# Optimization experiments

Measured on AMD Instinct MI355X. Metric: run time of the kernel, lower is better.

## Reference

```python
import jax, jax.numpy as jnp
import numpy as np

N_NODES = 50000
N_EDGES = 800000
D_IN = 128
D_H = 128
D_SIG = 16
D_OUT = 128


def _linear_params(key, fan_in, fan_out):
    kw, kb = jax.random.split(key)
    bound = 1.0 / np.sqrt(fan_in)
    w = jax.random.uniform(kw, (fan_in, fan_out), jnp.float32, -bound, bound)
    b = jax.random.uniform(kb, (fan_out,), jnp.float32, -bound, bound)
    return w, b


def setup_inputs() -> dict:
    key = jax.random.key(0)
    ks = jax.random.split(key, 7)
    x = jax.random.normal(ks[0], (N_NODES, D_IN), jnp.float32)
    edge_index = jax.random.randint(ks[1], (2, N_EDGES), 0, N_NODES, jnp.int64 if jax.config.jax_enable_x64 else jnp.int32)
    enc_w, enc_b = _linear_params(ks[2], D_IN, D_H)
    sig_w, sig_b = _linear_params(ks[3], D_H, D_SIG)
    msg_w, msg_b = _linear_params(ks[4], D_H, D_H)
    agg_w, agg_b = _linear_params(ks[5], 2 * D_H, D_H)
    dec_w, dec_b = _linear_params(ks[6], D_H, D_OUT)
    return {"x": x, "edge_index": edge_index,
            "enc_w": enc_w, "enc_b": enc_b,
            "sig_w": sig_w, "sig_b": sig_b,
            "msg_w": msg_w, "msg_b": msg_b,
            "agg_w": agg_w, "agg_b": agg_b,
            "dec_w": dec_w, "dec_b": dec_b}


def reference(x, edge_index, enc_w, enc_b, sig_w, sig_b, msg_w, msg_b, agg_w, agg_b, dec_w, dec_b):
    n = x.shape[0]
    h = x @ enc_w + enc_b                                   # [N, D_H]
    sig = h @ sig_w + sig_b                                 # [N, D_SIG]
    # F.normalize: x / max(||x||_2, eps)
    sig = sig / jnp.maximum(jnp.linalg.norm(sig, axis=-1, keepdims=True), 1e-12)
    msg = jax.nn.relu(h @ msg_w + msg_b)                    # [N, D_H]

    src, dst = edge_index[0], edge_index[1]
    # per-edge signature dot product, then segment softmax over each src node's edges
    scores = jnp.sum(sig[src] * sig[dst], axis=-1)          # [E]
    smax = jax.ops.segment_max(scores, src, num_segments=n)
    smax = jnp.where(jnp.isfinite(smax), smax, 0.0)         # empty segments -> 0
    e = jnp.exp(scores - smax[src])
    denom = jax.ops.segment_sum(e, src, num_segments=n)
    w = e / denom[src]                                      # [E]
    # weighted message aggregation; nodes with no out-edges get zeros
    comm = jax.ops.segment_sum(w[:, None] * msg[dst], src, num_segments=n)  # [N, D_H]

    combined = jax.nn.relu(jnp.concatenate([h, comm], axis=-1) @ agg_w + agg_b)
    return combined @ dec_w + dec_b
```

## Files before the change

### kernel.cpp

```cpp
#include <hip/hip_runtime.h>
#include <math.h>

#define N_NODES 50000
#define N_EDGES 800000
#define CAP 64
#define NRANGE 782
#define PCAP 1280
#define EPBA 2560
#define NBA 313
#define NBE 391

typedef __attribute__((ext_vector_type(8)))  short s16x8;
typedef __attribute__((ext_vector_type(16))) float f32x16;
typedef unsigned int u32;
typedef unsigned short u16;

union U16B { uint4 u; s16x8 s; };

__device__ __forceinline__ u32 bfr(float f) {
    u32 u = __float_as_uint(f);
    return (u + 0x7FFFu + ((u >> 16) & 1u)) >> 16;
}
__device__ __forceinline__ u32 pkbf(float a, float b) { return bfr(a) | (bfr(b) << 16); }
__device__ __forceinline__ float bf2f(u32 b) { return __uint_as_float(b << 16); }
__device__ __forceinline__ float dotpair(u32 a, u32 b) {
    return bf2f(a & 0xFFFFu) * bf2f(b & 0xFFFFu) + bf2f(a >> 16) * bf2f(b >> 16);
}

__device__ __forceinline__ uint4 buildfrag(const float* d8, int hh) {
    u32 P = pkbf(d8[0], d8[1]), Q = pkbf(d8[2], d8[3]);
    u32 R = pkbf(d8[4], d8[5]), S = pkbf(d8[6], d8[7]);
    u32 sP = (u32)__shfl_xor((int)P, 32);
    u32 sQ = (u32)__shfl_xor((int)Q, 32);
    u32 sR = (u32)__shfl_xor((int)R, 32);
    u32 sS = (u32)__shfl_xor((int)S, 32);
    uint4 f;
    f.x = hh ? sR : P;  f.y = hh ? sS : Q;
    f.z = hh ? R : sP;  f.w = hh ? S : sQ;
    return f;
}
#define BUILDF(OUT, ACC, Q, HH) do { \
    float _td[8]; \
    _Pragma("unroll") for (int _z = 0; _z < 8; ++_z) _td[_z] = (ACC)[(Q)*8 + _z]; \
    (OUT) = buildfrag(_td, HH); } while (0)
#define BUILDR(OUT, ACC, Q, HH) do { \
    float _td[8]; \
    _Pragma("unroll") for (int _z = 0; _z < 8; ++_z) _td[_z] = fmaxf((ACC)[(Q)*8 + _z], 0.f); \
    (OUT) = buildfrag(_td, HH); } while (0)

__global__ __launch_bounds__(256) void k_prep(
    const float* __restrict__ enc_w, const float* __restrict__ msg_w,
    const float* __restrict__ sig_w, const float* __restrict__ agg_w,
    const float* __restrict__ dec_w,
    uint4* __restrict__ WtE, uint4* __restrict__ WtM, uint4* __restrict__ WtD,
    uint4* __restrict__ WtA0, uint4* __restrict__ WtA1, uint4* __restrict__ WtS,
    int* __restrict__ gcur)
{
    int gid = blockIdx.x * 256 + threadIdx.x;
    if (gid < NRANGE) gcur[gid] = 0;
    if (gid < 10240) {
        int m = gid >> 11, r = gid & 2047;
        int col = r >> 4, s = r & 15;
        const float* W; uint4* D; int kb = 0;
        if      (m == 0) { W = enc_w; D = WtE; }
        else if (m == 1) { W = msg_w; D = WtM; }
        else if (m == 2) { W = dec_w; D = WtD; }
        else if (m == 3) { W = agg_w; D = WtA0; }
        else             { W = agg_w; D = WtA1; kb = 128; }
        float v[8];
        #pragma unroll
        for (int j = 0; j < 8; ++j) v[j] = W[(size_t)(kb + s * 8 + j) * 128 + col];
        uint4 w;
        w.x = pkbf(v[0], v[1]); w.y = pkbf(v[2], v[3]);
        w.z = pkbf(v[4], v[5]); w.w = pkbf(v[6], v[7]);
        D[col * 16 + (s ^ (col & 7))] = w;
    } else if (gid < 10752) {
        int r = gid - 10240;
        int row = r >> 4, s = r & 15;
        float v[8];
        #pragma unroll
        for (int j = 0; j < 8; ++j)
            v[j] = (row < 16) ? sig_w[(size_t)(s * 8 + j) * 16 + row] : 0.0f;
        uint4 w;
        w.x = pkbf(v[0], v[1]); w.y = pkbf(v[2], v[3]);
        w.z = pkbf(v[4], v[5]); w.w = pkbf(v[6], v[7]);
        WtS[row * 16 + (s ^ (row & 7))] = w;
    }
}

__global__ __launch_bounds__(256) void k_enc_part(
    const float* __restrict__ x,
    const uint4* __restrict__ WtE, const uint4* __restrict__ WtM,
    const uint4* __restrict__ WtS,
    const float* __restrict__ enc_b, const float* __restrict__ sig_b,
    const float* __restrict__ msg_b,
    uint4* __restrict__ h_g, u32* __restrict__ sig_bf, uint4* __restrict__ msg_g,
    const int* __restrict__ src, const int* __restrict__ dst,
    int* __restrict__ gcur, u32* __restrict__ part)
{
    __shared__ uint4 LB[2048];
    __shared__ float LS[2176];

    const int t = threadIdx.x;

    if (blockIdx.x >= NBE) {
        int* hist = (int*)LB;
        int* base = hist + NRANGE;
        const int e0 = (blockIdx.x - NBE) * EPBA;
        for (int i = t; i < NRANGE; i += 256) hist[i] = 0;
        __syncthreads();
        #pragma unroll 4
        for (int k = 0; k < EPBA / 256; ++k) {
            int e = e0 + k * 256 + t;
            if (e < N_EDGES) atomicAdd(&hist[src[e] >> 6], 1);
        }
        __syncthreads();
        for (int i = t; i < NRANGE; i += 256) {
            int h = hist[i];
            base[i] = h ? atomicAdd(&gcur[i], h) : 0;
        }
        __syncthreads();
        for (int i = t; i < NRANGE; i += 256) hist[i] = 0;
        __syncthreads();
        #pragma unroll 4
        for (int k = 0; k < EPBA / 256; ++k) {
            int e = e0 + k * 256 + t;
            if (e < N_EDGES) {
                int s = src[e], d = dst[e];
                int r = s >> 6;
                int p = base[r] + atomicAdd(&hist[r], 1);
                part[(size_t)r * PCAP + p] = ((u32)s << 16) | (u32)d;
            }
        }
        return;
    }

    const int node0 = blockIdx.x * 128;
    int nrem = N_NODES - node0; if (nrem > 128) nrem = 128;
    const int lane = t & 63, wid = t >> 6;
    const int l31 = lane & 31, hh = lane >> 5;
    const int nloc = wid * 32 + l31;
    const int sw7 = l31 & 7;

    #pragma unroll
    for (int it = 0; it < 8; ++it) {
        int idx = it * 256 + t;
        int nd = idx >> 4, s = idx & 15;
        float4 v0 = make_float4(0, 0, 0, 0), v1 = v0;
        if (nd < nrem) {
            const float4* px = (const float4*)(x + (size_t)(node0 + nd) * 128 + s * 8);
            v0 = px[0]; v1 = px[1];
        }
        uint4 w;
        w.x = pkbf(v0.x, v0.y); w.y = pkbf(v0.z, v0.w);
        w.z = pkbf(v1.x, v1.y); w.w = pkbf(v1.z, v1.w);
        LB[nd * 16 + (s ^ (nd & 7))] = w;
    }
    __syncthreads();

    const char* lb = (const char*)LB;
    const char* gwE = (const char*)WtE;
    const char* gwM = (const char*)WtM;
    const char* gwS = (const char*)WtS;

    f32x16 a0 = {}, a1 = {}, a2 = {}, a3 = {};
    #pragma unroll
    for (int r = 0; r < 16; ++r) {
        int rr = (r & 3) + 8 * (r >> 2) + 4 * hh;
        a0[r] = enc_b[rr];      a1[r] = enc_b[32 + rr];
        a2[r] = enc_b[64 + rr]; a3[r] = enc_b[96 + rr];
    }
    #pragma unroll
    for (int ks = 0; ks < 8; ++ks) {
        int so = ((ks * 2 + hh) ^ sw7) << 4;
        s16x8 bf = *(const s16x8*)(lb + nloc * 256 + so);
        s16x8 w0 = *(const s16x8*)(gwE + l31 * 256 + so);
        s16x8 w1 = *(const s16x8*)(gwE + 8192 + l31 * 256 + so);
        s16x8 w2 = *(const s16x8*)(gwE + 16384 + l31 * 256 + so);
        s16x8 w3 = *(const s16x8*)(gwE + 24576 + l31 * 256 + so);
        a0 = __builtin_amdgcn_mfma_f32_32x32x16_bf16(w0, bf, a0, 0, 0, 0);
        a1 = __builtin_amdgcn_mfma_f32_32x32x16_bf16(w1, bf, a1, 0, 0, 0);
        a2 = __builtin_amdgcn_mfma_f32_32x32x16_bf16(w2, bf, a2, 0, 0, 0);
        a3 = __builtin_amdgcn_mfma_f32_32x32x16_bf16(w3, bf, a3, 0, 0, 0);
    }

    uint4 hf[8];
    BUILDF(hf[0], a0, 0, hh); BUILDF(hf[1], a0, 1, hh);
    BUILDF(hf[2], a1, 0, hh); BUILDF(hf[3], a1, 1, hh);
    BUILDF(hf[4], a2, 0, hh); BUILDF(hf[5], a2, 1, hh);
    BUILDF(hf[6], a3, 0, hh); BUILDF(hf[7], a3, 1, hh);

    __syncthreads();
    #pragma unroll
    for (int f = 0; f < 8; ++f) {
        int g = 2 * f + hh;
        LB[nloc * 16 + (g ^ sw7)] = hf[f];
    }

    f32x16 m0 = {}, m1 = {}, m2 = {}, m3 = {};
    #pragma unroll
    for (int r = 0; r < 16; ++r) {
        int rr = (r & 3) + 8 * (r >> 2) + 4 * hh;
        m0[r] = msg_b[rr];      m1[r] = msg_b[32 + rr];
        m2[r] = msg_b[64 + rr]; m3[r] = msg_b[96 + rr];
    }
    #pragma unroll
    for (int ks = 0; ks < 8; ++ks) {
        int so = ((ks * 2 + hh) ^ sw7) << 4;
        U16B hb; hb.u = hf[ks];
        s16x8 w0 = *(const s16x8*)(gwM + l31 * 256 + so);
        s16x8 w1 = *(const s16x8*)(gwM + 8192 + l31 * 256 + so);
        s16x8 w2 = *(const s16x8*)(gwM + 16384 + l31 * 256 + so);
        s16x8 w3 = *(const s16x8*)(gwM + 24576 + l31 * 256 + so);
        m0 = __builtin_amdgcn_mfma_f32_32x32x16_bf16(w0, hb.s, m0, 0, 0, 0);
        m1 = __builtin_amdgcn_mfma_f32_32x32x16_bf16(w1, hb.s, m1, 0, 0, 0);
        m2 = __builtin_amdgcn_mfma_f32_32x32x16_bf16(w2, hb.s, m2, 0, 0, 0);
        m3 = __builtin_amdgcn_mfma_f32_32x32x16_bf16(w3, hb.s, m3, 0, 0, 0);
    }
    uint4 mf[8];
    BUILDR(mf[0], m0, 0, hh); BUILDR(mf[1], m0, 1, hh);
    BUILDR(mf[2], m1, 0, hh); BUILDR(mf[3], m1, 1, hh);
    BUILDR(mf[4], m2, 0, hh); BUILDR(mf[5], m2, 1, hh);
    BUILDR(mf[6], m3, 0, hh); BUILDR(mf[7], m3, 1, hh);

    __syncthreads();
    #pragma unroll
    for (int it = 0; it < 8; ++it) {
        int idx = it * 256 + t;
        if ((idx >> 4) < nrem) h_g[(size_t)node0 * 16 + idx] = LB[idx];
    }
    __syncthreads();
    #pragma unroll
    for (int f = 0; f < 8; ++f)
        LB[nloc * 16 + 2 * f + hh] = mf[f];

    f32x16 sg = {};
    #pragma unroll
    for (int r = 0; r < 8; ++r) {
        int rr = (r & 3) + 8 * (r >> 2) + 4 * hh;
        sg[r] = sig_b[rr];
    }
    #pragma unroll
    for (int ks = 0; ks < 8; ++ks) {
        int so = ((ks * 2 + hh) ^ sw7) << 4;
        s16x8 aw = *(const s16x8*)(gwS + l31 * 256 + so);
        U16B hb; hb.u = hf[ks];
        sg = __builtin_amdgcn_mfma_f32_32x32x16_bf16(aw, hb.s, sg, 0, 0, 0);
    }
    float ss = 0.f;
    #pragma unroll
    for (int r = 0; r < 8; ++r) ss += sg[r] * sg[r];
    ss += __shfl_xor(ss, 32);
    float inv = 1.0f / fmaxf(sqrtf(ss), 1e-12f);
    #pragma unroll
    for (int r = 0; r < 8; ++r) {
        int sc = (r & 3) + 8 * (r >> 2) + 4 * hh;
        LS[nloc * 17 + sc] = sg[r] * inv;
    }
    __syncthreads();

    #pragma unroll
    for (int it = 0; it < 8; ++it) {
        int idx = it * 256 + t;
        if ((idx >> 4) < nrem) msg_g[(size_t)node0 * 16 + idx] = LB[idx];
    }
    #pragma unroll
    for (int it = 0; it < 4; ++it) {
        int idx = it * 256 + t;
        int nd = idx >> 3, c2 = idx & 7;
        if (nd < nrem)
            sig_bf[(size_t)(node0 + nd) * 8 + c2] =
                pkbf(LS[nd * 17 + 2 * c2], LS[nd * 17 + 2 * c2 + 1]);
    }
}

__global__ __launch_bounds__(256) void k_decode_m(
    const uint4* __restrict__ h_g, const uint4* __restrict__ comm,
    const uint4* __restrict__ WtA0, const uint4* __restrict__ WtA1,
    const uint4* __restrict__ WtD,
    const float* __restrict__ agg_b, const float* __restrict__ dec_b,
    float* __restrict__ out)
{
    __shared__ uint4 LB[2048];
    __shared__ uint4 LW[2048];

    const int t = threadIdx.x;
    const int node0 = blockIdx.x * 64;
    int nrem = N_NODES - node0; if (nrem > 64) nrem = 64;
    const int lane = t & 63, wid = t >> 6;
    const int l31 = lane & 31, hh = lane >> 5;
    const int ng = wid & 1, cp = wid >> 1;
    const int nloc = ng * 32 + l31;
    const int sw7 = l31 & 7;

    #pragma unroll
    for (int it = 0; it < 8; ++it) {
        int idx = it * 256 + t;
        int nd = idx >> 5, g = idx & 31;
        uint4 v = make_uint4(0, 0, 0, 0);
        if (nd < nrem)
            v = (g < 16) ? h_g[(size_t)(node0 + nd) * 16 + g]
                         : comm[(size_t)(node0 + nd) * 16 + (g - 16)];
        LB[nd * 32 + g] = v;
        LW[idx] = WtA0[idx];
    }
    __syncthreads();

    const char* lb = (const char*)LB;
    const char* lw = (const char*)LW;

    f32x16 c0 = {}, c1 = {};
    #pragma unroll
    for (int r = 0; r < 16; ++r) {
        int rr = (r & 3) + 8 * (r >> 2) + 4 * hh;
        c0[r] = agg_b[cp * 64 + rr];
        c1[r] = agg_b[cp * 64 + 32 + rr];
    }
    #pragma unroll
    for (int ks = 0; ks < 8; ++ks) {
        int so = ((ks * 2 + hh) ^ sw7) << 4;
        s16x8 bf = *(const s16x8*)(lb + nloc * 512 + so);
        s16x8 w0 = *(const s16x8*)(lw + (cp * 64 + l31) * 256 + so);
        s16x8 w1 = *(const s16x8*)(lw + (cp * 64 + 32 + l31) * 256 + so);
        c0 = __builtin_amdgcn_mfma_f32_32x32x16_bf16(w0, bf, c0, 0, 0, 0);
        c1 = __builtin_amdgcn_mfma_f32_32x32x16_bf16(w1, bf, c1, 0, 0, 0);
    }
    __syncthreads();
    #pragma unroll
    for (int it = 0; it < 8; ++it) LW[it * 256 + t] = WtA1[it * 256 + t];
    __syncthreads();
    #pragma unroll
    for (int ks = 8; ks < 16; ++ks) {
        int so = ((ks * 2 + hh) ^ sw7) << 4;
        int so2 = (((ks - 8) * 2 + hh) ^ sw7) << 4;
        s16x8 bf = *(const s16x8*)(lb + nloc * 512 + so);
        s16x8 w0 = *(const s16x8*)(lw + (cp * 64 + l31) * 256 + so2);
        s16x8 w1 = *(const s16x8*)(lw + (cp * 64 + 32 + l31) * 256 + so2);
        c0 = __builtin_amdgcn_mfma_f32_32x32x16_bf16(w0, bf, c0, 0, 0, 0);
        c1 = __builtin_amdgcn_mfma_f32_32x32x16_bf16(w1, bf, c1, 0, 0, 0);
    }
    __syncthreads();

    {
        uint4 cf[4];
        BUILDR(cf[0], c0, 0, hh); BUILDR(cf[1], c0, 1, hh);
        BUILDR(cf[2], c1, 0, hh); BUILDR(cf[3], c1, 1, hh);
        #pragma unroll
        for (int f = 0; f < 4; ++f) {
            int g = (cp * 4 + f) * 2 + hh;
            LB[nloc * 16 + (g ^ sw7)] = cf[f];
        }
    }
    #pragma unroll
    for (int it = 0; it < 8; ++it) LW[it * 256 + t] = WtD[it * 256 + t];
    __syncthreads();

    f32x16 o0 = {}, o1 = {};
    {
        float b0 = dec_b[cp * 64 + l31], b1 = dec_b[cp * 64 + 32 + l31];
        #pragma unroll
        for (int r = 0; r < 16; ++r) { o0[r] = b0; o1[r] = b1; }
    }
    #pragma unroll
    for (int ks = 0; ks < 8; ++ks) {
        int so = ((ks * 2 + hh) ^ sw7) << 4;
        s16x8 af = *(const s16x8*)(lb + nloc * 256 + so);
        s16x8 w0 = *(const s16x8*)(lw + (cp * 64 + l31) * 256 + so);
        s16x8 w1 = *(const s16x8*)(lw + (cp * 64 + 32 + l31) * 256 + so);
        o0 = __builtin_amdgcn_mfma_f32_32x32x16_bf16(af, w0, o0, 0, 0, 0);
        o1 = __builtin_amdgcn_mfma_f32_32x32x16_bf16(af, w1, o1, 0, 0, 0);
    }
    #pragma unroll
    for (int r = 0; r < 16; ++r) {
        int nd = ng * 32 + (r & 3) + 8 * (r >> 2) + 4 * hh;
        if (nd < nrem) {
            float* row = out + (size_t)(node0 + nd) * 128 + cp * 64;
            row[l31]      = o0[r];
            row[32 + l31] = o1[r];
        }
    }
}

__global__ __launch_bounds__(256) void k_pb_aggr(
    const int* __restrict__ gcur, const u32* __restrict__ part,
    const u32* __restrict__ sig_bf,
    const char* __restrict__ msg_g, char* __restrict__ comm)
{
    __shared__ int   cnt[64];
    __shared__ float lden[64];
    __shared__ int2  lde[64 * CAP];

    const int t = threadIdx.x;
    const int r = blockIdx.x;
    const int node0 = r * 64;

    if (t < 64) { cnt[t] = 0; lden[t] = 0.f; }
    __syncthreads();

    const int total = gcur[r];
    for (int i = t; i < total; i += 256) {
        u32 en = part[(size_t)r * PCAP + i];
        int s = (int)(en >> 16), d = (int)(en & 0xFFFFu);
        const uint4* ps = (const uint4*)(sig_bf + (size_t)s * 8);
        const uint4* pd = (const uint4*)(sig_bf + (size_t)d * 8);
        uint4 sa = ps[0], sb = ps[1];
        uint4 da = pd[0], db = pd[1];
        float dot = dotpair(sa.x, da.x) + dotpair(sa.y, da.y)
                  + dotpair(sa.z, da.z) + dotpair(sa.w, da.w)
                  + dotpair(sb.x, db.x) + dotpair(sb.y, db.y)
                  + dotpair(sb.z, db.z) + dotpair(sb.w, db.w);
        float e = __expf(dot);
        int sl = s & 63;
        int p = atomicAdd(&cnt[sl], 1);
        lde[sl * CAP + p] = make_int2(d, __float_as_int(e));
        atomicAdd(&lden[sl], e);
    }
    __syncthreads();

    const int lane = t & 63, wid = t >> 6;
    const int l31 = lane & 31, hh = lane >> 5;
    #pragma unroll
    for (int g = 0; g < 8; ++g) {
        const int nloc = wid * 16 + 2 * g + hh;
        const int node = node0 + nloc;
        const int cn = cnt[nloc];
        const int2* ld = &lde[nloc * CAP];
        float a0 = 0.f, a1 = 0.f, a2 = 0.f, a3 = 0.f;
        int k = 0;
        for (; k + 4 <= cn; k += 4) {
            int2 d0 = ld[k], d1 = ld[k + 1], d2 = ld[k + 2], d3 = ld[k + 3];
            uint2 m0 = *(const uint2*)(msg_g + (size_t)d0.x * 256 + 8 * l31);
            uint2 m1 = *(const uint2*)(msg_g + (size_t)d1.x * 256 + 8 * l31);
            uint2 m2 = *(const uint2*)(msg_g + (size_t)d2.x * 256 + 8 * l31);
            uint2 m3 = *(const uint2*)(msg_g + (size_t)d3.x * 256 + 8 * l31);
            float e0 = __int_as_float(d0.y), e1 = __int_as_float(d1.y);
            float e2 = __int_as_float(d2.y), e3 = __int_as_float(d3.y);
            a0 += e0 * bf2f(m0.x & 0xFFFFu); a1 += e0 * bf2f(m0.x >> 16);
            a2 += e0 * bf2f(m0.y & 0xFFFFu); a3 += e0 * bf2f(m0.y >> 16);
            a0 += e1 * bf2f(m1.x & 0xFFFFu); a1 += e1 * bf2f(m1.x >> 16);
            a2 += e1 * bf2f(m1.y & 0xFFFFu); a3 += e1 * bf2f(m1.y >> 16);
            a0 += e2 * bf2f(m2.x & 0xFFFFu); a1 += e2 * bf2f(m2.x >> 16);
            a2 += e2 * bf2f(m2.y & 0xFFFFu); a3 += e2 * bf2f(m2.y >> 16);
            a0 += e3 * bf2f(m3.x & 0xFFFFu); a1 += e3 * bf2f(m3.x >> 16);
            a2 += e3 * bf2f(m3.y & 0xFFFFu); a3 += e3 * bf2f(m3.y >> 16);
        }
        for (; k < cn; ++k) {
            int2 de = ld[k];
            float e = __int_as_float(de.y);
            uint2 m = *(const uint2*)(msg_g + (size_t)de.x * 256 + 8 * l31);
            a0 += e * bf2f(m.x & 0xFFFFu);
            a1 += e * bf2f(m.x >> 16);
            a2 += e * bf2f(m.y & 0xFFFFu);
            a3 += e * bf2f(m.y >> 16);
        }
        float den = lden[nloc];
        float inv = (den > 0.f) ? (1.0f / den) : 0.f;
        if (node < N_NODES) {
            uint2 w;
            w.x = pkbf(a0 * inv, a1 * inv);
            w.y = pkbf(a2 * inv, a3 * inv);
            *(uint2*)(comm + (size_t)node * 256 + ((8 * l31) ^ ((node & 7) << 4))) = w;
        }
    }
}

extern "C" void kernel_launch(void* const* d_in, const int* in_sizes, int n_in,
                              void* d_out, int out_size, void* d_ws, size_t ws_size,
                              hipStream_t stream)
{
    const float* x     = (const float*)d_in[0];
    const int*   ei    = (const int*)  d_in[1];
    const float* enc_w = (const float*)d_in[2];
    const float* enc_b = (const float*)d_in[3];
    const float* sig_w = (const float*)d_in[4];
    const float* sig_b = (const float*)d_in[5];
    const float* msg_w = (const float*)d_in[6];
    const float* msg_b = (const float*)d_in[7];
    const float* agg_w = (const float*)d_in[8];
    const float* agg_b = (const float*)d_in[9];
    const float* dec_w = (const float*)d_in[10];
    const float* dec_b = (const float*)d_in[11];
    float* out = (float*)d_out;

    const int* src = ei;
    const int* dst = ei + N_EDGES;

    char* p = (char*)d_ws;
    uint4* h_g   = (uint4*)p;  p += (size_t)N_NODES * 256;
    uint4* msg_g = (uint4*)p;  p += (size_t)N_NODES * 256;
    uint4* comm  = (uint4*)p;  p += (size_t)N_NODES * 256;
    u32*   sig_bf = (u32*)p;   p += (size_t)N_NODES * 32;
    u32*   part   = (u32*)p;   p += (size_t)NRANGE * PCAP * 4;
    int*   gcur   = (int*)p;   p += 4096;
    uint4* WtE  = (uint4*)p; p += 32768;
    uint4* WtM  = (uint4*)p; p += 32768;
    uint4* WtD  = (uint4*)p; p += 32768;
    uint4* WtA0 = (uint4*)p; p += 32768;
    uint4* WtA1 = (uint4*)p; p += 32768;
    uint4* WtS  = (uint4*)p; p += 8192;

    k_prep<<<42, 256, 0, stream>>>(enc_w, msg_w, sig_w, agg_w, dec_w,
                                   WtE, WtM, WtD, WtA0, WtA1, WtS, gcur);
    k_enc_part<<<NBE + NBA, 256, 0, stream>>>(
        x, WtE, WtM, WtS, enc_b, sig_b, msg_b, h_g, sig_bf, msg_g,
        src, dst, gcur, part);
    k_pb_aggr<<<NRANGE, 256, 0, stream>>>(
        gcur, part, sig_bf, (const char*)msg_g, (char*)comm);
    k_decode_m<<<(N_NODES + 63) / 64, 256, 0, stream>>>(
        h_g, comm, WtA0, WtA1, WtD, agg_b, dec_b, out);
}
```

Before: 95.60 us.

## Split encoder tile across waves by output columns, halving nodes per block

The encoder/message/signature block now handles 64 nodes instead of 128. Its four waves are split into two node groups times two column halves, so each wave computes 64 output channels instead of 128. This doubles the number of node blocks, halves per-wave accumulator registers and LDS use, and is meant to raise occupancy and parallelism. In exchange, the message GEMM now reloads h from LDS instead of registers, adds an extra barrier, and leaves half the waves idle during the signature GEMM.

Measured after the change: 97.06 us. No clear change (+1.5%).

```diff
diff --git a/kernel.cpp b/kernel.cpp
--- a/kernel.cpp
+++ b/kernel.cpp
@@ -8,7 +8,7 @@
 #define PCAP 1280
 #define EPBA 2560
 #define NBA 313
-#define NBE 391
+#define NBE 782
 
 typedef __attribute__((ext_vector_type(8)))  short s16x8;
 typedef __attribute__((ext_vector_type(16))) float f32x16;
@@ -98,8 +98,8 @@
     const int* __restrict__ src, const int* __restrict__ dst,
     int* __restrict__ gcur, u32* __restrict__ part)
 {
-    __shared__ uint4 LB[2048];
-    __shared__ float LS[2176];
+    __shared__ uint4 LB[1024];
+    __shared__ float LS[1088];
 
     const int t = threadIdx.x;
 
@@ -135,15 +135,18 @@
         return;
     }
 
-    const int node0 = blockIdx.x * 128;
-    int nrem = N_NODES - node0; if (nrem > 128) nrem = 128;
+    const int node0 = blockIdx.x * 64;
+    int nrem = N_NODES - node0; if (nrem > 64) nrem = 64;
     const int lane = t & 63, wid = t >> 6;
     const int l31 = lane & 31, hh = lane >> 5;
-    const int nloc = wid * 32 + l31;
+    const int ng = wid & 1;
+    const int ch = wid >> 1;
+    const int nloc = ng * 32 + l31;
     const int sw7 = l31 & 7;
-
-    #pragma unroll
-    for (int it = 0; it < 8; ++it) {
+    const int cb = ch * 64;
+
+    #pragma unroll
+    for (int it = 0; it < 4; ++it) {
         int idx = it * 256 + t;
         int nd = idx >> 4, s = idx & 15;
         float4 v0 = make_float4(0, 0, 0, 0), v1 = v0;
@@ -163,109 +166,104 @@
     const char* gwM = (const char*)WtM;
     const char* gwS = (const char*)WtS;
 
-    f32x16 a0 = {}, a1 = {}, a2 = {}, a3 = {};
+    f32x16 a0 = {}, a1 = {};
     #pragma unroll
     for (int r = 0; r < 16; ++r) {
         int rr = (r & 3) + 8 * (r >> 2) + 4 * hh;
-        a0[r] = enc_b[rr];      a1[r] = enc_b[32 + rr];
-        a2[r] = enc_b[64 + rr]; a3[r] = enc_b[96 + rr];
+        a0[r] = enc_b[cb + rr];
+        a1[r] = enc_b[cb + 32 + rr];
     }
     #pragma unroll
     for (int ks = 0; ks < 8; ++ks) {
         int so = ((ks * 2 + hh) ^ sw7) << 4;
         s16x8 bf = *(const s16x8*)(lb + nloc * 256 + so);
-        s16x8 w0 = *(const s16x8*)(gwE + l31 * 256 + so);
-        s16x8 w1 = *(const s16x8*)(gwE + 8192 + l31 * 256 + so);
-        s16x8 w2 = *(const s16x8*)(gwE + 16384 + l31 * 256 + so);
-        s16x8 w3 = *(const s16x8*)(gwE + 24576 + l31 * 256 + so);
+        s16x8 w0 = *(const s16x8*)(gwE + (cb + l31) * 256 + so);
+        s16x8 w1 = *(const s16x8*)(gwE + (cb + 32 + l31) * 256 + so);
         a0 = __builtin_amdgcn_mfma_f32_32x32x16_bf16(w0, bf, a0, 0, 0, 0);
         a1 = __builtin_amdgcn_mfma_f32_32x32x16_bf16(w1, bf, a1, 0, 0, 0);
-        a2 = __builtin_amdgcn_mfma_f32_32x32x16_bf16(w2, bf, a2, 0, 0, 0);
-        a3 = __builtin_amdgcn_mfma_f32_32x32x16_bf16(w3, bf, a3, 0, 0, 0);
-    }
-
-    uint4 hf[8];
+    }
+
+    uint4 hf[4];
     BUILDF(hf[0], a0, 0, hh); BUILDF(hf[1], a0, 1, hh);
     BUILDF(hf[2], a1, 0, hh); BUILDF(hf[3], a1, 1, hh);
-    BUILDF(hf[4], a2, 0, hh); BUILDF(hf[5], a2, 1, hh);
-    BUILDF(hf[6], a3, 0, hh); BUILDF(hf[7], a3, 1, hh);
-
-    __syncthreads();
-    #pragma unroll
-    for (int f = 0; f < 8; ++f) {
-        int g = 2 * f + hh;
-        LB[nloc * 16 + (g ^ sw7)] = hf[f];
-    }
-
-    f32x16 m0 = {}, m1 = {}, m2 = {}, m3 = {};
+
+    __syncthreads();
+    #pragma unroll
+    for (int f = 0; f < 2; ++f) {
+        int g0 = ch * 8 + 2 * f + hh;
+        int g1 = ch * 8 + 4 + 2 * f + hh;
+        LB[nloc * 16 + (g0 ^ sw7)] = hf[f];
+        LB[nloc * 16 + (g1 ^ sw7)] = hf[2 + f];
+    }
+    __syncthreads();
+
+    f32x16 m0 = {}, m1 = {};
     #pragma unroll
     for (int r = 0; r < 16; ++r) {
         int rr = (r & 3) + 8 * (r >> 2) + 4 * hh;
-        m0[r] = msg_b[rr];      m1[r] = msg_b[32 + rr];
-        m2[r] = msg_b[64 + rr]; m3[r] = msg_b[96 + rr];
+        m0[r] = msg_b[cb + rr];
+        m1[r] = msg_b[cb + 32 + rr];
     }
     #pragma unroll
     for (int ks = 0; ks < 8; ++ks) {
         int so = ((ks * 2 + hh) ^ sw7) << 4;
-        U16B hb; hb.u = hf[ks];
-        s16x8 w0 = *(const s16x8*)(gwM + l31 * 256 + so);
-        s16x8 w1 = *(const s16x8*)(gwM + 8192 + l31 * 256 + so);
-        s16x8 w2 = *(const s16x8*)(gwM + 16384 + l31 * 256 + so);
-        s16x8 w3 = *(const s16x8*)(gwM + 24576 + l31 * 256 + so);
-        m0 = __builtin_amdgcn_mfma_f32_32x32x16_bf16(w0, hb.s, m0, 0, 0, 0);
-        m1 = __builtin_amdgcn_mfma_f32_32x32x16_bf16(w1, hb.s, m1, 0, 0, 0);
-        m2 = __builtin_amdgcn_mfma_f32_32x32x16_bf16(w2, hb.s, m2, 0, 0, 0);
-        m3 = __builtin_amdgcn_mfma_f32_32x32x16_bf16(w3, hb.s, m3, 0, 0, 0);
-    }
-    uint4 mf[8];
+        s16x8 bf = *(const s16x8*)(lb + nloc * 256 + so);
+        s16x8 w0 = *(const s16x8*)(gwM + (cb + l31) * 256 + so);
+        s16x8 w1 = *(const s16x8*)(gwM + (cb + 32 + l31) * 256 + so);
+        m0 = __builtin_amdgcn_mfma_f32_32x32x16_bf16(w0, bf, m0, 0, 0, 0);
+        m1 = __builtin_amdgcn_mfma_f32_32x32x16_bf16(w1, bf, m1, 0, 0, 0);
+    }
+    uint4 mf[4];
     BUILDR(mf[0], m0, 0, hh); BUILDR(mf[1], m0, 1, hh);
     BUILDR(mf[2], m1, 0, hh); BUILDR(mf[3], m1, 1, hh);
-    BUILDR(mf[4], m2, 0, hh); BUILDR(mf[5], m2, 1, hh);
-    BUILDR(mf[6], m3, 0, hh); BUILDR(mf[7], m3, 1, hh);
-
-    __syncthreads();
-    #pragma unroll
-    for (int it = 0; it < 8; ++it) {
+
+    if (ch == 0) {
+        f32x16 sg = {};
+        #pragma unroll
+        for (int r = 0; r < 8; ++r) {
+            int rr = (r & 3) + 8 * (r >> 2) + 4 * hh;
+            sg[r] = sig_b[rr];
+        }
+        #pragma unroll
+        for (int ks = 0; ks < 8; ++ks) {
+            int so = ((ks * 2 + hh) ^ sw7) << 4;
+            s16x8 bf = *(const s16x8*)(lb + nloc * 256 + so);
+            s16x8 aw = *(const s16x8*)(gwS + l31 * 256 + so);
+            sg = __builtin_amdgcn_mfma_f32_32x32x16_bf16(aw, bf, sg, 0, 0, 0);
+        }
+        float ss = 0.f;
+        #pragma unroll
+        for (int r = 0; r < 8; ++r) ss += sg[r] * sg[r];
+        ss += __shfl_xor(ss, 32);
+        float inv = 1.0f / fmaxf(sqrtf(ss), 1e-12f);
+        #pragma unroll
+        for (int r = 0; r < 8; ++r) {
+            int sc = (r & 3) + 8 * (r >> 2) + 4 * hh;
+            LS[nloc * 17 + sc] = sg[r] * inv;
+        }
+    }
+
+    #pragma unroll
+    for (int it = 0; it < 4; ++it) {
         int idx = it * 256 + t;
         if ((idx >> 4) < nrem) h_g[(size_t)node0 * 16 + idx] = LB[idx];
     }
     __syncthreads();
-    #pragma unroll
-    for (int f = 0; f < 8; ++f)
-        LB[nloc * 16 + 2 * f + hh] = mf[f];
-
-    f32x16 sg = {};
-    #pragma unroll
-    for (int r = 0; r < 8; ++r) {
-        int rr = (r & 3) + 8 * (r >> 2) + 4 * hh;
-        sg[r] = sig_b[rr];
-    }
-    #pragma unroll
-    for (int ks = 0; ks < 8; ++ks) {
-        int so = ((ks * 2 + hh) ^ sw7) << 4;
-        s16x8 aw = *(const s16x8*)(gwS + l31 * 256 + so);
-        U16B hb; hb.u = hf[ks];
-        sg = __builtin_amdgcn_mfma_f32_32x32x16_bf16(aw, hb.s, sg, 0, 0, 0);
-    }
-    float ss = 0.f;
-    #pragma unroll
-    for (int r = 0; r < 8; ++r) ss += sg[r] * sg[r];
-    ss += __shfl_xor(ss, 32);
-    float inv = 1.0f / fmaxf(sqrtf(ss), 1e-12f);
-    #pragma unroll
-    for (int r = 0; r < 8; ++r) {
-        int sc = (r & 3) + 8 * (r >> 2) + 4 * hh;
-        LS[nloc * 17 + sc] = sg[r] * inv;
-    }
-    __syncthreads();
-
-    #pragma unroll
-    for (int it = 0; it < 8; ++it) {
+
+    #pragma unroll
+    for (int f = 0; f < 2; ++f) {
+        LB[nloc * 16 + cb / 8 + 2 * f + hh]     = mf[f];
+        LB[nloc * 16 + cb / 8 + 4 + 2 * f + hh] = mf[2 + f];
+    }
+    __syncthreads();
+
+    #pragma unroll
+    for (int it = 0; it < 4; ++it) {
         int idx = it * 256 + t;
         if ((idx >> 4) < nrem) msg_g[(size_t)node0 * 16 + idx] = LB[idx];
     }
     #pragma unroll
-    for (int it = 0; it < 4; ++it) {
+    for (int it = 0; it < 2; ++it) {
         int idx = it * 256 + t;
         int nd = idx >> 3, c2 = idx & 7;
         if (nd < nrem)
```
